# Optimization experiments

Hardware: AMD Instinct MI355X
Metric: run time of the kernel (lower is better)

## Reference

```python
import jax, jax.numpy as jnp
import numpy as np

B, S, E, H = 4, 1024, 512, 8
DK = E // H


def setup_inputs() -> dict:
    key = jax.random.key(0)
    ks = jax.random.split(key, 16)
    s = 1.0 / np.sqrt(E)
    inp = {
        "query": jax.random.normal(ks[0], (B, S, E), dtype=jnp.float32),
        "key": jax.random.normal(ks[1], (B, S, E), dtype=jnp.float32),
        "value": jax.random.normal(ks[2], (B, S, E), dtype=jnp.float32),
        "dist_conv": jax.random.uniform(ks[3], (B, S, S), dtype=jnp.float32),
        "mask": jax.random.randint(ks[4], (B, S, S), 0, 2, dtype=jnp.int32),
        # four Linear(E, E) layers: q, k, v, out (torch: y = x @ W.T + b)
        "Wq": jax.random.normal(ks[5], (E, E), dtype=jnp.float32) * s,
        "bq": jnp.zeros((E,), dtype=jnp.float32),
        "Wk": jax.random.normal(ks[6], (E, E), dtype=jnp.float32) * s,
        "bk": jnp.zeros((E,), dtype=jnp.float32),
        "Wv": jax.random.normal(ks[7], (E, E), dtype=jnp.float32) * s,
        "bv": jnp.zeros((E,), dtype=jnp.float32),
        "Wo": jax.random.normal(ks[8], (E, E), dtype=jnp.float32) * s,
        "bo": jnp.zeros((E,), dtype=jnp.float32),
        # 1x1 Conv2d(1, H) -> ReLU -> 1x1 Conv2d(H, H)
        "cw1": jax.random.normal(ks[9], (H,), dtype=jnp.float32),  # [out_c] (in_c=1, k=1)
        "cb1": jnp.zeros((H,), dtype=jnp.float32),
        "cw2": jax.random.normal(ks[10], (H, H), dtype=jnp.float32) * (1.0 / np.sqrt(H)),
        "cb2": jnp.zeros((H,), dtype=jnp.float32),
    }
    return inp


def reference(query, key, value, dist_conv, mask, Wq, bq, Wk, bk, Wv, bv, Wo, bo, cw1, cb1, cw2, cb2):
    # projections, split into heads: [B, H, S, DK]
    def proj(x, W, b):
        y = jnp.einsum("bse,fe->bsf", x, W) + b
        return y.reshape(B, S, H, DK).transpose(0, 2, 1, 3)

    q = proj(query, Wq, bq)
    k = proj(key, Wk, bk)
    v = proj(value, Wv, bv)

    # 1x1 conv stack on distance matrix: [B,S,S] -> [B,H,S,S]
    t = jax.nn.relu(dist_conv[:, None] * cw1[None, :, None, None] + cb1[None, :, None, None])
    bias = jnp.einsum("bhij,gh->bgij", t, cw2) + cb2[None, :, None, None]

    scores = jnp.einsum("bhqd,bhkd->bhqk", q, k) / jnp.sqrt(jnp.float32(DK))
    scores = scores * bias
    scores = jnp.where(mask[:, None] == 0, jnp.float32(-1e9), scores)
    p_attn = jax.nn.softmax(scores, axis=-1)

    x = jnp.einsum("bhqk,bhkd->bhqd", p_attn, v)
    x = x.transpose(0, 2, 1, 3).reshape(B, S, E)
    return jnp.einsum("bse,fe->bsf", x, Wo) + bo
```

## Files before the change

kernel.cpp:

```cpp
#include <hip/hip_runtime.h>
#include <hip/hip_bf16.h>
#include <math.h>

#define B_ 4
#define S_ 1024
#define E_ 512
#define H_ 8
#define DK_ 64

typedef short bf16x8 __attribute__((ext_vector_type(8)));
typedef float f32x4 __attribute__((ext_vector_type(4)));

#define MFMA16(a, b, c) __builtin_amdgcn_mfma_f32_16x16x32_bf16((a), (b), (c), 0, 0, 0)
#define cfence() asm volatile("" ::: "memory")

__device__ __forceinline__ void gl_lds16(const void* gptr, void* lptr) {
    __builtin_amdgcn_global_load_lds(
        (const __attribute__((address_space(1))) unsigned int*)gptr,
        (__attribute__((address_space(3))) unsigned int*)lptr,
        16, 0, 0);
}

__device__ __forceinline__ unsigned short bf16_bits(float v) {
    __hip_bfloat16 h = __float2bfloat16(v);
    return *(unsigned short*)&h;
}

__global__ __launch_bounds__(256) void prep(
    const float* __restrict__ q, const float* __restrict__ k, const float* __restrict__ v,
    const float* __restrict__ wq, const float* __restrict__ wk,
    const float* __restrict__ wv, const float* __restrict__ wo,
    const float* __restrict__ dist, const int* __restrict__ mask,
    __hip_bfloat16* qc, __hip_bfloat16* kc, __hip_bfloat16* vc,
    __hip_bfloat16* wqc, __hip_bfloat16* wkc, __hip_bfloat16* wvc, __hip_bfloat16* woc,
    __hip_bfloat16* __restrict__ dM) {
    const int blk = blockIdx.x;
    const int tid = threadIdx.x;
    if (blk >= 3584) {
        const int bi = blk - 3584;
        const size_t E = (size_t)bi * 2048 + (size_t)tid * 8;
        const size_t R = E & ~(size_t)1023;
        const int po = (int)(E & 1023);
        const int itb = po >> 6;
        const int p = po & 63;
        const int g = p >> 4, tth = (p >> 3) & 1;
        const int C = itb * 64 + tth * 32 + g * 4;
        float4 dA = *(const float4*)(dist + R + C);
        float4 dB = *(const float4*)(dist + R + C + 16);
        int4 mA = *(const int4*)(mask + R + C);
        int4 mB = *(const int4*)(mask + R + C + 16);
        float dv[8] = {dA.x, dA.y, dA.z, dA.w, dB.x, dB.y, dB.z, dB.w};
        int mv[8] = {mA.x, mA.y, mA.z, mA.w, mB.x, mB.y, mB.z, mB.w};
        union { unsigned short us[8]; uint4 u4; } o;
#pragma unroll
        for (int j = 0; j < 8; ++j) {
            unsigned short u = bf16_bits(dv[j]);
            if (mv[j] == 0) u = 0xFF80u;
            o.us[j] = u;
        }
        *(uint4*)(dM + E) = o.u4;
        return;
    }
    const float* src;
    __hip_bfloat16* dst;
    int base;
    if (blk < 1024)      { src = q; dst = qc; base = blk; }
    else if (blk < 2048) { src = k; dst = kc; base = blk - 1024; }
    else if (blk < 3072) { src = v; dst = vc; base = blk - 2048; }
    else {
        const int wz = (blk - 3072) >> 7;
        base = (blk - 3072) & 127;
        switch (wz) {
            case 0: src = wq; dst = wqc; break;
            case 1: src = wk; dst = wkc; break;
            case 2: src = wv; dst = wvc; break;
            default: src = wo; dst = woc; break;
        }
    }
    const int idx = (base * 256 + tid) * 8;
    float4 a = *(const float4*)(src + idx);
    float4 bb = *(const float4*)(src + idx + 4);
    union { __hip_bfloat16 h[8]; uint4 u; } o;
    o.h[0] = __float2bfloat16(a.x);  o.h[1] = __float2bfloat16(a.y);
    o.h[2] = __float2bfloat16(a.z);  o.h[3] = __float2bfloat16(a.w);
    o.h[4] = __float2bfloat16(bb.x); o.h[5] = __float2bfloat16(bb.y);
    o.h[6] = __float2bfloat16(bb.z); o.h[7] = __float2bfloat16(bb.w);
    *(uint4*)(dst + idx) = o.u;
}

template <int MT, int NROWS_W, int NT>
__device__ __forceinline__ void gemm_core64(const __hip_bfloat16* A, const __hip_bfloat16* W,
                                            char* sA, char* sW, int m0, int n0,
                                            f32x4 acc[MT][NT]) {
    const int t = threadIdx.x;
    const int w = t >> 6, lane = t & 63;
    const int wm = (w >> 1) * (MT * 16), wn = (w & 1) * (NT * 16);
    const int g = lane >> 4, ln = lane & 15;
    const int AB = MT * 4096;
    const int WB = NROWS_W * 128;

    const char* aaddr[MT];
    const char* waddr[NROWS_W / 32];
#pragma unroll
    for (int i = 0; i < MT; ++i) {
        int L = (i * 4 + w) * 64 + lane;
        int r = L >> 3, cs = L & 7;
        int c = cs ^ (r & 7);
        aaddr[i] = (const char*)A + (size_t)(m0 + r) * 1024 + c * 16;
    }
#pragma unroll
    for (int i = 0; i < NROWS_W / 32; ++i) {
        int L = (i * 4 + w) * 64 + lane;
        int r = L >> 3, cs = L & 7;
        int c = cs ^ (r & 7);
        waddr[i] = (const char*)W + (size_t)(n0 + r) * 1024 + c * 16;
    }

#pragma unroll
    for (int i = 0; i < MT; ++i) {
        gl_lds16(aaddr[i], sA + (i * 4 + w) * 1024);
        aaddr[i] += 128;
    }
#pragma unroll
    for (int i = 0; i < NROWS_W / 32; ++i) {
        gl_lds16(waddr[i], sW + (i * 4 + w) * 1024);
        waddr[i] += 128;
    }

    for (int kc = 0; kc < 8; ++kc) {
        const int cur = kc & 1;
        __syncthreads();
        if (kc < 7) {
            char* nA = sA + (cur ^ 1) * AB;
            char* nW = sW + (cur ^ 1) * WB;
#pragma unroll
            for (int i = 0; i < MT; ++i) {
                gl_lds16(aaddr[i], nA + (i * 4 + w) * 1024);
                aaddr[i] += 128;
            }
#pragma unroll
            for (int i = 0; i < NROWS_W / 32; ++i) {
                gl_lds16(waddr[i], nW + (i * 4 + w) * 1024);
                waddr[i] += 128;
            }
        }
        const char* cA = sA + cur * AB;
        const char* cW = sW + cur * WB;
#pragma unroll
        for (int ks = 0; ks < 2; ++ks) {
            bf16x8 af[MT], bf[NT];
#pragma unroll
            for (int mt = 0; mt < MT; ++mt) {
                int m = wm + mt * 16 + ln;
                int c = ks * 4 + g;
                af[mt] = *(const bf16x8*)(cA + m * 128 + (c ^ (m & 7)) * 16);
            }
#pragma unroll
            for (int nt = 0; nt < NT; ++nt) {
                int n = wn + nt * 16 + ln;
                int c = ks * 4 + g;
                bf[nt] = *(const bf16x8*)(cW + n * 128 + (c ^ (n & 7)) * 16);
            }
#pragma unroll
            for (int mt = 0; mt < MT; ++mt)
#pragma unroll
                for (int nt = 0; nt < NT; ++nt)
                    acc[mt][nt] = MFMA16(af[mt], bf[nt], acc[mt][nt]);
        }
    }
}

__global__ __launch_bounds__(256) void proj_gemm(
    const __hip_bfloat16* __restrict__ qc, const __hip_bfloat16* __restrict__ kc,
    const __hip_bfloat16* __restrict__ vc,
    const __hip_bfloat16* __restrict__ wqc, const __hip_bfloat16* __restrict__ wkc,
    const __hip_bfloat16* __restrict__ wvc,
    const float* __restrict__ bq, const float* __restrict__ bk, const float* __restrict__ bv,
    __hip_bfloat16* qbh, __hip_bfloat16* kbh, __hip_bfloat16* vt) {
    __shared__ char smem[49152];
    char* sA = smem;
    char* sW = smem + 16384;

    const int bid = blockIdx.x;
    const int tile = (bid & 7) * 96 + (bid >> 3);
    const int z = tile >> 8;
    const int rem = tile & 255;
    const int m0 = (rem >> 2) * 64;
    const int n0 = (rem & 3) * 128;

    const __hip_bfloat16* A;
    const __hip_bfloat16* W;
    const float* bias;
    __hip_bfloat16* dst;
    float scale;
    if (z == 0)      { A = qc; W = wqc; bias = bq; dst = qbh; scale = 0.125f; }
    else if (z == 1) { A = kc; W = wkc; bias = bk; dst = kbh; scale = 1.f; }
    else             { A = vc; W = wvc; bias = bv; dst = vt;  scale = 1.f; }

    f32x4 acc[2][4] = {};
    gemm_core64<2, 128, 4>(A, W, sA, sW, m0, n0, acc);
    __syncthreads();

    const int t = threadIdx.x;
    const int w = t >> 6, lane = t & 63;
    const int wm = (w >> 1) * 32, wn = (w & 1) * 64;
    const int g = lane >> 4, ln = lane & 15;
    const int b = m0 >> 10;
    float bv4[4];
#pragma unroll
    for (int nt = 0; nt < 4; ++nt) bv4[nt] = bias[n0 + wn + nt * 16 + ln];

    __hip_bfloat16* T = (__hip_bfloat16*)smem;
    if (z != 2) {
#pragma unroll
        for (int mt = 0; mt < 2; ++mt)
#pragma unroll
            for (int nt = 0; nt < 4; ++nt)
#pragma unroll
                for (int r = 0; r < 4; ++r)
                    T[(wm + mt * 16 + g * 4 + r) * 136 + wn + nt * 16 + ln] =
                        __float2bfloat16((acc[mt][nt][r] + bv4[nt]) * scale);
        __syncthreads();
        const int row = t >> 2, quarter = t & 3;
        const char* srow = (const char*)T + row * 272 + quarter * 64;
        const int s = (m0 & 1023) + row;
        const int h = (n0 >> 6) + (quarter >> 1);
        char* gdst = (char*)dst +
                     (((size_t)(b * 8 + h) * 1024 + s) * 64 + (quarter & 1) * 32) * 2;
#pragma unroll
        for (int j = 0; j < 4; ++j)
            *(uint4*)(gdst + j * 16) = *(const uint4*)(srow + j * 16);
    } else {
#pragma unroll
        for (int mt = 0; mt < 2; ++mt)
#pragma unroll
            for (int nt = 0; nt < 4; ++nt)
#pragma unroll
                for (int r = 0; r < 4; ++r)
                    T[(wm + mt * 16 + g * 4 + r) * 129 + wn + nt * 16 + ln] =
                        __float2bfloat16(acc[mt][nt][r] + bv4[nt]);
        __syncthreads();
        const int c = t >> 1, sel = t & 1;
        union { __hip_bfloat16 hh[32]; uint4 u[4]; } P;
#pragma unroll
        for (int i = 0; i < 32; ++i)
            P.hh[i] = T[(sel * 32 + i) * 129 + c];
        const int h = (n0 >> 6) + (c >> 6), dkk = c & 63;
        char* gdst = (char*)vt +
                     (((size_t)(b * 8 + h) * 64 + dkk) * 1024 + (m0 & 1023) + sel * 32) * 2;
#pragma unroll
        for (int j = 0; j < 4; ++j)
            *(uint4*)(gdst + j * 16) = P.u[j];
    }
}

__global__ __launch_bounds__(256) void out_gemm(
    const __hip_bfloat16* __restrict__ X, const __hip_bfloat16* __restrict__ woc,
    const float* __restrict__ bo, float* __restrict__ out) {
    __shared__ char smem[32768];
    char* sA = smem;
    char* sW = smem + 16384;

    const int bid = blockIdx.x;
    const int tile = (bid & 7) * 64 + (bid >> 3);
    const int m0 = (tile >> 3) * 64;
    const int n0 = (tile & 7) * 64;

    f32x4 acc[2][2] = {};
    gemm_core64<2, 64, 2>(X, woc, sA, sW, m0, n0, acc);

    const int t = threadIdx.x;
    const int w = t >> 6, lane = t & 63;
    const int wm = (w >> 1) * 32, wn = (w & 1) * 32;
    const int g = lane >> 4, ln = lane & 15;
    float bv2[2];
#pragma unroll
    for (int nt = 0; nt < 2; ++nt) bv2[nt] = bo[n0 + wn + nt * 16 + ln];
#pragma unroll
    for (int mt = 0; mt < 2; ++mt)
#pragma unroll
        for (int nt = 0; nt < 2; ++nt)
#pragma unroll
            for (int r = 0; r < 4; ++r) {
                int m = m0 + wm + mt * 16 + g * 4 + r;
                int f = n0 + wn + nt * 16 + ln;
                out[(size_t)m * 512 + f] = acc[mt][nt][r] + bv2[nt];
            }
}

__global__ __launch_bounds__(256) void attn_one(
    const __hip_bfloat16* __restrict__ Qb, const __hip_bfloat16* __restrict__ Kb,
    const __hip_bfloat16* __restrict__ Vt, const __hip_bfloat16* __restrict__ dM,
    const float* __restrict__ cw1, const float* __restrict__ cb1,
    const float* __restrict__ cw2, const float* __restrict__ cb2,
    __hip_bfloat16* __restrict__ X) {
    __shared__ char sK[2][8192];
    __shared__ char sV[2][8192];
    __shared__ __hip_bfloat16 sP[4][16 * 72];

    const int t = threadIdx.x, w = t >> 6, lane = t & 63;
    const int g = lane >> 4, ln = lane & 15;
    const int wg = blockIdx.x;
    const int xcd = wg & 7, sub = wg >> 3;
    const int bh = xcd * 4 + (sub >> 4);
    const int q0 = (sub & 15) * 64;

    char* sp = (char*)sP[w];

    const int gh = bh & 7;
    float Pc = 0.f, Cc = cb2[gh];
#pragma unroll
    for (int h = 0; h < 8; ++h) {
        float w2 = cw2[gh * 8 + h];
        Pc = fmaf(w2, fmaxf(cw1[h], 0.f), Pc);
        Cc = fmaf(w2, fmaxf(cb1[h], 0.f), Cc);
    }
    const float LOG2E = 1.4426950408889634f;
    Pc *= LOG2E; Cc *= LOG2E;

    bf16x8 qf[2];
    {
        const char* qbase = (const char*)Qb + ((size_t)bh * 1024 + q0 + w * 16 + ln) * 128;
        qf[0] = *(const bf16x8*)(qbase + g * 16);
        qf[1] = *(const bf16x8*)(qbase + 64 + g * 16);
    }

    const char* kaddr[2];
    const char* vaddr[2];
#pragma unroll
    for (int i = 0; i < 2; ++i) {
        int L = (i * 4 + w) * 64 + lane;
        int r = L >> 3, cs = L & 7;
        int c = cs ^ (r & 7);
        kaddr[i] = (const char*)Kb + (size_t)bh * 131072 + (size_t)r * 128 + c * 16;
        vaddr[i] = (const char*)Vt + (size_t)bh * 131072 + (size_t)r * 2048 + c * 16;
    }
    const char* daddr = (const char*)dM +
        (((size_t)(bh >> 3) * 1024 + q0 + w * 16 + ln) * 1024 + g * 16) * 2;

    float m_st = -1e30f, l_st = 0.f;
    f32x4 O[4] = {};

#pragma unroll
    for (int i = 0; i < 2; ++i) {
        gl_lds16(kaddr[i], sK[0] + (i * 4 + w) * 1024);
        gl_lds16(vaddr[i], sV[0] + (i * 4 + w) * 1024);
        kaddr[i] += 8192;
        vaddr[i] += 128;
    }
    uint4 dnA = *(const uint4*)(daddr);
    uint4 dnB = *(const uint4*)(daddr + 16);
    daddr += 128;

    for (int it = 0; it < 16; ++it) {
        const int cur = it & 1;
        __syncthreads();
        uint4 dA = dnA, dB = dnB;
        if (it < 15) {
#pragma unroll
            for (int i = 0; i < 2; ++i) {
                gl_lds16(kaddr[i], sK[cur ^ 1] + (i * 4 + w) * 1024);
                gl_lds16(vaddr[i], sV[cur ^ 1] + (i * 4 + w) * 1024);
                kaddr[i] += 8192;
                vaddr[i] += 128;
            }
            dnA = *(const uint4*)(daddr);
            dnB = *(const uint4*)(daddr + 16);
            daddr += 128;
        }

        f32x4 scv[4] = {};
#pragma unroll
        for (int tt = 0; tt < 4; ++tt)
#pragma unroll
            for (int ks = 0; ks < 2; ++ks) {
                int key = tt * 16 + ln;
                int cc = ks * 4 + g;
                bf16x8 kf = *(const bf16x8*)(sK[cur] + key * 128 + (cc ^ (key & 7)) * 16);
                scv[tt] = MFMA16(kf, qf[ks], scv[tt]);
            }

        unsigned int wds[8] = {dA.x, dA.y, dA.z, dA.w, dB.x, dB.y, dB.z, dB.w};
        float s2[16];
#pragma unroll
        for (int m = 0; m < 16; ++m) {
            unsigned int bits = (m & 1) ? (wds[m >> 1] & 0xFFFF0000u)
                                        : (wds[m >> 1] << 16);
            float f = fmaf(__uint_as_float(bits), Pc, Cc);
            float s = scv[m >> 2][m & 3] * f;
            s = (bits == 0xFF800000u) ? -1e9f : s;
            s2[m] = s;
        }
        float t8[8];
#pragma unroll
        for (int j = 0; j < 8; ++j) t8[j] = fmaxf(s2[2 * j], s2[2 * j + 1]);
        float t4a = fmaxf(t8[0], t8[1]), t4b = fmaxf(t8[2], t8[3]);
        float t4c = fmaxf(t8[4], t8[5]), t4d = fmaxf(t8[6], t8[7]);
        float mx = fmaxf(fmaxf(t4a, t4b), fmaxf(t4c, t4d));
        mx = fmaxf(mx, __shfl_xor(mx, 16));
        mx = fmaxf(mx, __shfl_xor(mx, 32));

        const bool full = __any(mx > m_st + 8.f);
        float alpha = 1.f;
        if (full) {
            const float mnew = fmaxf(m_st, mx);
            alpha = __builtin_amdgcn_exp2f(m_st - mnew);
            m_st = mnew;
        }
        float pv16[16];
#pragma unroll
        for (int i = 0; i < 16; ++i) pv16[i] = __builtin_amdgcn_exp2f(s2[i] - m_st);
        float r8[8];
#pragma unroll
        for (int j = 0; j < 8; ++j) r8[j] = pv16[2 * j] + pv16[2 * j + 1];
        float r4a = r8[0] + r8[1], r4b = r8[2] + r8[3];
        float r4c = r8[4] + r8[5], r4d = r8[6] + r8[7];
        float rs = (r4a + r4b) + (r4c + r4d);
        rs += __shfl_xor(rs, 16);
        rs += __shfl_xor(rs, 32);
        l_st = (full ? l_st * alpha : l_st) + rs;

#pragma unroll
        for (int tt = 0; tt < 4; ++tt) {
            union { unsigned short u[4]; uint2 v; } pk;
            pk.u[0] = bf16_bits(pv16[tt * 4 + 0]);
            pk.u[1] = bf16_bits(pv16[tt * 4 + 1]);
            pk.u[2] = bf16_bits(pv16[tt * 4 + 2]);
            pk.u[3] = bf16_bits(pv16[tt * 4 + 3]);
            *(uint2*)(sp + ln * 144 + tt * 32 + g * 8) = pk.v;
        }
        cfence();

        if (full) {
            float al4[4];
#pragma unroll
            for (int rr = 0; rr < 4; ++rr)
                al4[rr] = __shfl(alpha, (lane & 48) + g * 4 + rr);
#pragma unroll
            for (int tt = 0; tt < 4; ++tt)
#pragma unroll
                for (int rr = 0; rr < 4; ++rr) O[tt][rr] *= al4[rr];
        }

#pragma unroll
        for (int ks = 0; ks < 2; ++ks) {
            bf16x8 pf = *(const bf16x8*)(sp + ln * 144 + ks * 64 + g * 16);
#pragma unroll
            for (int tt = 0; tt < 4; ++tt) {
                int dk = tt * 16 + ln;
                int cc = ks * 4 + g;
                bf16x8 vf = *(const bf16x8*)(sV[cur] + dk * 128 + (cc ^ (dk & 7)) * 16);
                O[tt] = MFMA16(pf, vf, O[tt]);
            }
        }
        cfence();
    }

    const float inv = 1.f / l_st;
    float iv4[4];
#pragma unroll
    for (int rr = 0; rr < 4; ++rr)
        iv4[rr] = __shfl(inv, (lane & 48) + g * 4 + rr);
    const int b = bh >> 3, h = bh & 7;
#pragma unroll
    for (int rr = 0; rr < 4; ++rr) {
        const int s = q0 + w * 16 + g * 4 + rr;
        __hip_bfloat16* xrow = X + ((size_t)(b * 1024 + s)) * 512 + h * 64;
#pragma unroll
        for (int tt = 0; tt < 4; ++tt)
            xrow[tt * 16 + ln] = __float2bfloat16(O[tt][rr] * iv4[rr]);
    }
}

extern "C" void kernel_launch(void* const* d_in, const int* in_sizes, int n_in,
                              void* d_out, int out_size, void* d_ws, size_t ws_size,
                              hipStream_t stream) {
    (void)in_sizes; (void)n_in; (void)out_size; (void)ws_size;
    const float* query = (const float*)d_in[0];
    const float* key   = (const float*)d_in[1];
    const float* value = (const float*)d_in[2];
    const float* dist  = (const float*)d_in[3];
    const int*   mask  = (const int*)d_in[4];
    const float* Wq = (const float*)d_in[5];
    const float* bq = (const float*)d_in[6];
    const float* Wk = (const float*)d_in[7];
    const float* bk = (const float*)d_in[8];
    const float* Wv = (const float*)d_in[9];
    const float* bv = (const float*)d_in[10];
    const float* Wo = (const float*)d_in[11];
    const float* bo = (const float*)d_in[12];
    const float* cw1 = (const float*)d_in[13];
    const float* cb1 = (const float*)d_in[14];
    const float* cw2 = (const float*)d_in[15];
    const float* cb2 = (const float*)d_in[16];
    float* out = (float*)d_out;

    char* ws = (char*)d_ws;
    const size_t MB = 1 << 20;
    __hip_bfloat16* qc  = (__hip_bfloat16*)(ws + 0 * MB);
    __hip_bfloat16* kc  = (__hip_bfloat16*)(ws + 4 * MB);
    __hip_bfloat16* vc  = (__hip_bfloat16*)(ws + 8 * MB);
    __hip_bfloat16* wqc = (__hip_bfloat16*)(ws + 12 * MB);
    __hip_bfloat16* wkc = (__hip_bfloat16*)(ws + 12 * MB + 512 * 1024);
    __hip_bfloat16* wvc = (__hip_bfloat16*)(ws + 13 * MB);
    __hip_bfloat16* woc = (__hip_bfloat16*)(ws + 13 * MB + 512 * 1024);
    __hip_bfloat16* qbh = (__hip_bfloat16*)(ws + 14 * MB);
    __hip_bfloat16* kbh = (__hip_bfloat16*)(ws + 18 * MB);
    __hip_bfloat16* vt  = (__hip_bfloat16*)(ws + 22 * MB);
    __hip_bfloat16* x   = (__hip_bfloat16*)(ws + 26 * MB);
    __hip_bfloat16* dMp = (__hip_bfloat16*)(ws + 32 * MB);

    hipLaunchKernelGGL(prep, dim3(5632), dim3(256), 0, stream,
                       query, key, value, Wq, Wk, Wv, Wo, dist, mask,
                       qc, kc, vc, wqc, wkc, wvc, woc, dMp);
    hipLaunchKernelGGL(proj_gemm, dim3(768), dim3(256), 0, stream,
                       qc, kc, vc, wqc, wkc, wvc, bq, bk, bv, qbh, kbh, vt);
    hipLaunchKernelGGL(attn_one, dim3(512), dim3(256), 0, stream,
                       qbh, kbh, vt, dMp, cw1, cb1, cw2, cb2, x);
    hipLaunchKernelGGL(out_gemm, dim3(512), dim3(256), 0, stream,
                       x, woc, bo, out);
}
```

Before: 171.7 us.

## Split attention over key halves and merge partial results in a combine kernel

```diff
diff --git a/kernel.cpp b/kernel.cpp
--- a/kernel.cpp
+++ b/kernel.cpp
@@ -288,12 +288,12 @@
             }
 }
 
-__global__ __launch_bounds__(256) void attn_one(
+__global__ __launch_bounds__(256) void attn_split(
     const __hip_bfloat16* __restrict__ Qb, const __hip_bfloat16* __restrict__ Kb,
     const __hip_bfloat16* __restrict__ Vt, const __hip_bfloat16* __restrict__ dM,
     const float* __restrict__ cw1, const float* __restrict__ cb1,
     const float* __restrict__ cw2, const float* __restrict__ cb2,
-    __hip_bfloat16* __restrict__ X) {
+    __hip_bfloat16* __restrict__ Op, float2* __restrict__ Ml) {
     __shared__ char sK[2][8192];
     __shared__ char sV[2][8192];
     __shared__ __hip_bfloat16 sP[4][16 * 72];
@@ -302,8 +302,11 @@
     const int g = lane >> 4, ln = lane & 15;
     const int wg = blockIdx.x;
     const int xcd = wg & 7, sub = wg >> 3;
-    const int bh = xcd * 4 + (sub >> 4);
-    const int q0 = (sub & 15) * 64;
+    const int bh = xcd * 4 + (sub >> 5);
+    const int rem = sub & 31;
+    const int q0 = (rem >> 1) * 64;
+    const int spl = rem & 1;
+    const int kt0 = spl * 512;
 
     char* sp = (char*)sP[w];
 
@@ -332,11 +335,11 @@
         int L = (i * 4 + w) * 64 + lane;
         int r = L >> 3, cs = L & 7;
         int c = cs ^ (r & 7);
-        kaddr[i] = (const char*)Kb + (size_t)bh * 131072 + (size_t)r * 128 + c * 16;
-        vaddr[i] = (const char*)Vt + (size_t)bh * 131072 + (size_t)r * 2048 + c * 16;
+        kaddr[i] = (const char*)Kb + (size_t)bh * 131072 + (size_t)(kt0 + r) * 128 + c * 16;
+        vaddr[i] = (const char*)Vt + (size_t)bh * 131072 + (size_t)r * 2048 + (size_t)kt0 * 2 + c * 16;
     }
     const char* daddr = (const char*)dM +
-        (((size_t)(bh >> 3) * 1024 + q0 + w * 16 + ln) * 1024 + g * 16) * 2;
+        (((size_t)(bh >> 3) * 1024 + q0 + w * 16 + ln) * 1024 + kt0 + g * 16) * 2;
 
     float m_st = -1e30f, l_st = 0.f;
     f32x4 O[4] = {};
@@ -352,11 +355,11 @@
     uint4 dnB = *(const uint4*)(daddr + 16);
     daddr += 128;
 
-    for (int it = 0; it < 16; ++it) {
+    for (int it = 0; it < 8; ++it) {
         const int cur = it & 1;
         __syncthreads();
         uint4 dA = dnA, dB = dnB;
-        if (it < 15) {
+        if (it < 7) {
 #pragma unroll
             for (int i = 0; i < 2; ++i) {
                 gl_lds16(kaddr[i], sK[cur ^ 1] + (i * 4 + w) * 1024);
@@ -370,6 +373,7 @@
         }
 
         f32x4 scv[4] = {};
+        __builtin_amdgcn_s_setprio(1);
 #pragma unroll
         for (int tt = 0; tt < 4; ++tt)
 #pragma unroll
@@ -379,6 +383,7 @@
                 bf16x8 kf = *(const bf16x8*)(sK[cur] + key * 128 + (cc ^ (key & 7)) * 16);
                 scv[tt] = MFMA16(kf, qf[ks], scv[tt]);
             }
+        __builtin_amdgcn_s_setprio(0);
 
         unsigned int wds[8] = {dA.x, dA.y, dA.z, dA.w, dB.x, dB.y, dB.z, dB.w};
         float s2[16];
@@ -442,6 +447,7 @@
                 for (int rr = 0; rr < 4; ++rr) O[tt][rr] *= al4[rr];
         }
 
+        __builtin_amdgcn_s_setprio(1);
 #pragma unroll
         for (int ks = 0; ks < 2; ++ks) {
             bf16x8 pf = *(const bf16x8*)(sp + ln * 144 + ks * 64 + g * 16);
@@ -453,23 +459,45 @@
                 O[tt] = MFMA16(pf, vf, O[tt]);
             }
         }
+        __builtin_amdgcn_s_setprio(0);
         cfence();
     }
 
-    const float inv = 1.f / l_st;
-    float iv4[4];
-#pragma unroll
-    for (int rr = 0; rr < 4; ++rr)
-        iv4[rr] = __shfl(inv, (lane & 48) + g * 4 + rr);
-    const int b = bh >> 3, h = bh & 7;
+    const size_t rowbase = ((size_t)spl * 32 + bh) * 1024 + q0 + w * 16;
+    if (lane < 16) {
+        float2 ml2; ml2.x = m_st; ml2.y = l_st;
+        Ml[rowbase + ln] = ml2;
+    }
 #pragma unroll
     for (int rr = 0; rr < 4; ++rr) {
-        const int s = q0 + w * 16 + g * 4 + rr;
-        __hip_bfloat16* xrow = X + ((size_t)(b * 1024 + s)) * 512 + h * 64;
+        const int qrow = g * 4 + rr;
 #pragma unroll
         for (int tt = 0; tt < 4; ++tt)
-            xrow[tt * 16 + ln] = __float2bfloat16(O[tt][rr] * iv4[rr]);
-    }
+            Op[(rowbase + qrow) * 64 + tt * 16 + ln] = __float2bfloat16(O[tt][rr]);
+    }
+}
+
+__global__ __launch_bounds__(256) void combine(
+    const __hip_bfloat16* __restrict__ Op, const float2* __restrict__ Ml,
+    __hip_bfloat16* __restrict__ X) {
+    const int idx = blockIdx.x * 256 + threadIdx.x;
+    const int row = idx >> 5;
+    const int pr = (idx & 31) * 2;
+    float2 ml1 = Ml[row], ml2 = Ml[32768 + row];
+    float m = fmaxf(ml1.x, ml2.x);
+    float w1 = __builtin_amdgcn_exp2f(ml1.x - m), w2 = __builtin_amdgcn_exp2f(ml2.x - m);
+    float inv = 1.f / fmaf(ml1.y, w1, ml2.y * w2);
+    unsigned int u1 = *(const unsigned int*)(Op + (size_t)row * 64 + pr);
+    unsigned int u2 = *(const unsigned int*)(Op + ((size_t)32768 + row) * 64 + pr);
+    float o1x = __uint_as_float(u1 << 16), o1y = __uint_as_float(u1 & 0xFFFF0000u);
+    float o2x = __uint_as_float(u2 << 16), o2y = __uint_as_float(u2 & 0xFFFF0000u);
+    float x0 = fmaf(o1x, w1, o2x * w2) * inv;
+    float x1 = fmaf(o1y, w1, o2y * w2) * inv;
+    const int bh = row >> 10, s = row & 1023, b = bh >> 3, h = bh & 7;
+    union { __hip_bfloat16 hh[2]; unsigned int u; } o;
+    o.hh[0] = __float2bfloat16(x0);
+    o.hh[1] = __float2bfloat16(x1);
+    *(unsigned int*)(X + ((size_t)(b * 1024 + s)) * 512 + h * 64 + pr) = o.u;
 }
 
 extern "C" void kernel_launch(void* const* d_in, const int* in_sizes, int n_in,
@@ -509,14 +537,17 @@
     __hip_bfloat16* vt  = (__hip_bfloat16*)(ws + 22 * MB);
     __hip_bfloat16* x   = (__hip_bfloat16*)(ws + 26 * MB);
     __hip_bfloat16* dMp = (__hip_bfloat16*)(ws + 32 * MB);
+    __hip_bfloat16* Op  = (__hip_bfloat16*)(ws + 96 * MB);
+    float2*         Ml  = (float2*)(ws + 112 * MB);
 
     hipLaunchKernelGGL(prep, dim3(5632), dim3(256), 0, stream,
                        query, key, value, Wq, Wk, Wv, Wo, dist, mask,
                        qc, kc, vc, wqc, wkc, wvc, woc, dMp);
     hipLaunchKernelGGL(proj_gemm, dim3(768), dim3(256), 0, stream,
                        qc, kc, vc, wqc, wkc, wvc, bq, bk, bv, qbh, kbh, vt);
-    hipLaunchKernelGGL(attn_one, dim3(512), dim3(256), 0, stream,
-                       qbh, kbh, vt, dMp, cw1, cb1, cw2, cb2, x);
+    hipLaunchKernelGGL(attn_split, dim3(1024), dim3(256), 0, stream,
+                       qbh, kbh, vt, dMp, cw1, cb1, cw2, cb2, Op, Ml);
+    hipLaunchKernelGGL(combine, dim3(4096), dim3(256), 0, stream, Op, Ml, x);
     hipLaunchKernelGGL(out_gemm, dim3(512), dim3(256), 0, stream,
                        x, woc, bo, out);
 }
```

Measured after the change: 177.8 us. +3.5%, slower.
